# Kernel tuning notes

Hardware: AMD Instinct MI355X
Metric: run time of the kernel (lower is better)

Reference implementation:

```python
import jax, jax.numpy as jnp
import numpy as np

N_NODES = 50000


def gcn_conv(x, src, dst, deg_inv_sqrt, W, b, n_nodes):
    # GCNConv: h = x @ W; msg = norm * h[src]; out = scatter_add(msg, dst) + b
    h = x @ W  # [N, out]
    norm = deg_inv_sqrt[src] * deg_inv_sqrt[dst]  # symmetric normalization
    msg = h[src] * norm[:, None]  # [E+N, out]
    out = jax.ops.segment_sum(msg, dst, num_segments=n_nodes)
    return out + b


def setup_inputs() -> dict:
    key = jax.random.key(0)
    k_x, k_e, k_w1, k_w2 = jax.random.split(key, 4)
    in_c, hid, out_c = 256, 64, 64
    x = jax.random.normal(k_x, (N_NODES, 256), dtype=jnp.float32)
    edge_index = jax.random.randint(k_e, (2, 1600000), 0, N_NODES, dtype=jnp.int64)
    # Glorot-ish weights, zero bias as in GCNConv defaults
    W1 = jax.random.normal(k_w1, (in_c, hid), dtype=jnp.float32) / np.sqrt(in_c)
    b1 = jnp.zeros((hid,), dtype=jnp.float32)
    W2 = jax.random.normal(k_w2, (hid, out_c), dtype=jnp.float32) / np.sqrt(hid)
    b2 = jnp.zeros((out_c,), dtype=jnp.float32)
    return {"x": x, "edge_index": edge_index, "W1": W1, "b1": b1, "W2": W2, "b2": b2}


def reference(x, edge_index, W1, b1, W2, b2):
    n = x.shape[0]
    loops = jnp.arange(n, dtype=edge_index.dtype)
    src = jnp.concatenate([edge_index[0], loops])  # add self-loops
    dst = jnp.concatenate([edge_index[1], loops])
    deg = jax.ops.segment_sum(jnp.ones_like(dst, dtype=x.dtype), dst, num_segments=n)
    deg_inv_sqrt = jnp.where(deg > 0, jax.lax.rsqrt(deg), 0.0)
    h = gcn_conv(x, src, dst, deg_inv_sqrt, W1, b1, n)
    h = jax.nn.relu(h)
    out = gcn_conv(h, src, dst, deg_inv_sqrt, W2, b2, n)
    return out
```

## Files before the change

kernel.cpp:

```cpp
#include <hip/hip_runtime.h>
#include <hip/hip_bf16.h>


#define NB_MAX 1024

__device__ inline unsigned short f2bf(float f) {
    unsigned u = __builtin_bit_cast(unsigned, f);
    return (unsigned short)((u + 0x7FFFu + ((u >> 16) & 1u)) >> 16);
}
__device__ inline float bf2f(unsigned short b) {
    return __builtin_bit_cast(float, (unsigned)b << 16);
}


__global__ __launch_bounds__(256) void k_hist(const int* __restrict__ ei, int E,
                                              int nb, int chunk,
                                              int* __restrict__ histT) {
    __shared__ int h[NB_MAX];
    for (int i = threadIdx.x; i < nb; i += 256) h[i] = 0;
    __syncthreads();
    int e0 = blockIdx.x * chunk, e1 = min(E, e0 + chunk);
    for (int e = e0 + threadIdx.x; e < e1; e += 256)
        atomicAdd(&h[ei[E + e] >> 6], 1);
    __syncthreads();
    for (int b = threadIdx.x; b < nb; b += 256)
        histT[b * 256 + blockIdx.x] = h[b];
}


__global__ __launch_bounds__(256) void k_scan_cols(int* __restrict__ histT,
                                                   int* __restrict__ total) {
    __shared__ int sm[256];
    int b = blockIdx.x, t = threadIdx.x;
    int v = histT[b * 256 + t];
    sm[t] = v;
    __syncthreads();
    for (int off = 1; off < 256; off <<= 1) {
        int u = (t >= off) ? sm[t - off] : 0;
        __syncthreads();
        sm[t] += u;
        __syncthreads();
    }
    histT[b * 256 + t] = sm[t] - v;
    if (t == 255) total[b] = sm[255];
}


__global__ __launch_bounds__(1024) void k_scan_totals(const int* __restrict__ total,
                                                      int* __restrict__ base, int nb) {
    __shared__ int sm[1024];
    int t = threadIdx.x;
    int v = (t < nb) ? total[t] : 0;
    sm[t] = v;
    __syncthreads();
    for (int off = 1; off < 1024; off <<= 1) {
        int u = (t >= off) ? sm[t - off] : 0;
        __syncthreads();
        sm[t] += u;
        __syncthreads();
    }
    if (t < nb) base[t] = sm[t] - v;
    if (t == nb - 1) base[nb] = sm[t];
}


__global__ __launch_bounds__(256) void k_scatter(const int* __restrict__ ei, int E,
                                                 int nb, int chunk,
                                                 const int* __restrict__ histT,
                                                 const int* __restrict__ base,
                                                 unsigned* __restrict__ packed) {
    __shared__ int cur[NB_MAX];
    for (int b = threadIdx.x; b < nb; b += 256)
        cur[b] = base[b] + histT[b * 256 + blockIdx.x];
    __syncthreads();
    int e0 = blockIdx.x * chunk, e1 = min(E, e0 + chunk);
    for (int e = e0 + threadIdx.x; e < e1; e += 256) {
        int s = ei[e], d = ei[E + e];
        int pos = atomicAdd(&cur[d >> 6], 1);
        packed[pos] = (unsigned)s | ((unsigned)(d & 63) << 16);
    }
}


__global__ __launch_bounds__(256) void k_csr(const unsigned* __restrict__ packed,
                                             const int* __restrict__ base,
                                             int n,
                                             int* __restrict__ qbeg,
                                             int* __restrict__ qcnt,
                                             float* __restrict__ dinv,
                                             unsigned short* __restrict__ ssrcp,
                                             unsigned short* __restrict__ hs1,
                                             unsigned short* __restrict__ hs2) {
    __shared__ int cnt[64];
    __shared__ int cur[64];
    const int b = blockIdx.x, t = threadIdx.x;
    const int p0 = base[b], p1 = base[b + 1];
    if (t < 64) cnt[t] = 0;
    __syncthreads();
    for (int p = p0 + t; p < p1; p += 256)
        atomicAdd(&cnt[(packed[p] >> 16) & 63], 1);
    __syncthreads();
    if (t < 64) {
        int deg = cnt[t];
        int pdeg = (deg + 1) & ~1;
        int sum = pdeg;
#pragma unroll
        for (int d = 1; d < 64; d <<= 1) {
            int u = __shfl_up(sum, d, 64);
            if (t >= d) sum += u;
        }
        int excl = sum - pdeg;
        int pb = (2 + p0 + 128 * b + 1) & ~1;
        int start = pb + excl;
        int node = (b << 6) + t;
        if (node < n) {
            qbeg[node] = start >> 1;
            qcnt[node] = pdeg >> 1;
            dinv[node] = 1.0f / sqrtf((float)(deg + 1));
        }
        cur[t] = start;
    }
    __syncthreads();
    for (int p = p0 + t; p < p1; p += 256) {
        unsigned k = packed[p];
        int pos = atomicAdd(&cur[(k >> 16) & 63], 1);
        ssrcp[pos] = (unsigned short)(k & 0xFFFFu);
    }
    __syncthreads();
    if (t < 64 && (cnt[t] & 1))
        ssrcp[cur[t]] = (unsigned short)n;
    if (b == 0) {
        if (t < 64) {
            hs1[(size_t)n * 64 + t] = 0;
            hs2[(size_t)n * 64 + t] = 0;
        }
        if (t == 0) {
            ssrcp[0] = (unsigned short)n;
            ssrcp[1] = (unsigned short)n;
        }
    }
}


#define FMA4(A, s, wv)                                                         \
    (A).x += (s) * (wv).x; (A).y += (s) * (wv).y;                              \
    (A).z += (s) * (wv).z; (A).w += (s) * (wv).w;

template <int K>
__global__ __launch_bounds__(256) void k_gemm(const float* __restrict__ X,
                                              const float* __restrict__ W,
                                              const float* __restrict__ dinv,
                                              unsigned short* __restrict__ HS,
                                              int n) {
    __shared__ float xl[64][36];
    __shared__ float wl[32][64];

    const int t = threadIdx.x;
    const int tc = t & 15;
    const int tr = t >> 4;
    const int row0 = blockIdx.x * 64;

    float4 acc[4];
    acc[0] = acc[1] = acc[2] = acc[3] = make_float4(0.f, 0.f, 0.f, 0.f);

    for (int k0 = 0; k0 < K; k0 += 32) {
#pragma unroll
        for (int i = 0; i < 2; ++i) {
            int idx = i * 256 + t;
            int r = idx >> 3, f4 = idx & 7;
            int gr = row0 + r;
            float4 v = make_float4(0.f, 0.f, 0.f, 0.f);
            if (gr < n) v = *(const float4*)(X + (size_t)gr * K + k0 + f4 * 4);
            *(float4*)&xl[r][f4 * 4] = v;
        }
#pragma unroll
        for (int i = 0; i < 2; ++i) {
            int idx = i * 256 + t;
            int kr = idx >> 4, f4 = idx & 15;
            *(float4*)&wl[kr][f4 * 4] =
                *(const float4*)(W + (size_t)(k0 + kr) * 64 + f4 * 4);
        }
        __syncthreads();

#pragma unroll
        for (int kk = 0; kk < 32; kk += 4) {
            float4 xv0 = *(float4*)&xl[tr * 4 + 0][kk];
            float4 xv1 = *(float4*)&xl[tr * 4 + 1][kk];
            float4 xv2 = *(float4*)&xl[tr * 4 + 2][kk];
            float4 xv3 = *(float4*)&xl[tr * 4 + 3][kk];
            float4 wv0 = *(float4*)&wl[kk + 0][tc * 4];
            float4 wv1 = *(float4*)&wl[kk + 1][tc * 4];
            float4 wv2 = *(float4*)&wl[kk + 2][tc * 4];
            float4 wv3 = *(float4*)&wl[kk + 3][tc * 4];

            FMA4(acc[0], xv0.x, wv0); FMA4(acc[0], xv0.y, wv1);
            FMA4(acc[0], xv0.z, wv2); FMA4(acc[0], xv0.w, wv3);
            FMA4(acc[1], xv1.x, wv0); FMA4(acc[1], xv1.y, wv1);
            FMA4(acc[1], xv1.z, wv2); FMA4(acc[1], xv1.w, wv3);
            FMA4(acc[2], xv2.x, wv0); FMA4(acc[2], xv2.y, wv1);
            FMA4(acc[2], xv2.z, wv2); FMA4(acc[2], xv2.w, wv3);
            FMA4(acc[3], xv3.x, wv0); FMA4(acc[3], xv3.y, wv1);
            FMA4(acc[3], xv3.z, wv2); FMA4(acc[3], xv3.w, wv3);
        }
        __syncthreads();
    }

#pragma unroll
    for (int ri = 0; ri < 4; ++ri) {
        int gr = row0 + tr * 4 + ri;
        if (gr < n) {
            float dv = dinv[gr];
            float4 o = acc[ri];
            ushort4 pk;
            pk.x = f2bf(o.x * dv); pk.y = f2bf(o.y * dv);
            pk.z = f2bf(o.z * dv); pk.w = f2bf(o.w * dv);
            *(ushort4*)(HS + (size_t)gr * 64 + tc * 4) = pk;
        }
    }
}


template <bool RELU>
__global__ void k_agg(const unsigned short* __restrict__ hs,
                      const int* __restrict__ qbeg,
                      const int* __restrict__ qcnt,
                      const unsigned short* __restrict__ ssrcp,
                      const float* __restrict__ dinv,
                      const float* __restrict__ bias,
                      float* __restrict__ out, int n) {
    int node = blockIdx.x * 4 + (threadIdx.x >> 6);
    if (node >= n) return;
    node = __builtin_amdgcn_readfirstlane(node);
    const int lane = threadIdx.x & 63;
    const int half = lane >> 5;
    const int cp   = lane & 31;

    const unsigned* hsu = (const unsigned*)hs;
    const unsigned* ssu = (const unsigned*)ssrcp;

    const int q0 = qbeg[node];
    const int m  = qcnt[node];

    const unsigned sv = hsu[node * 32 + cp];
    const float dv = dinv[node];
    const float2 bv = *(const float2*)(bias + 2 * cp);

    float ax = 0.f, ay = 0.f;
    int qb = 0;
    for (; qb + 16 <= m; qb += 16) {
        unsigned ss[16];
#pragma unroll
        for (int j = 0; j < 16; ++j) ss[j] = ssu[q0 + qb + j];
        unsigned v[16];
#pragma unroll
        for (int j = 0; j < 16; ++j) {
            int s = half ? (int)(ss[j] >> 16) : (int)(ss[j] & 0xFFFFu);
            v[j] = hsu[s * 32 + cp];
        }
#pragma unroll
        for (int j = 0; j < 16; ++j) {
            ax += __builtin_bit_cast(float, v[j] << 16);
            ay += __builtin_bit_cast(float, v[j] & 0xFFFF0000u);
        }
    }
    const int rem = m - qb;
    if (rem) {
        unsigned ss[16];
#pragma unroll
        for (int j = 0; j < 16; ++j) {
            int q = (j < rem) ? (q0 + qb + j) : 0;
            ss[j] = ssu[q];
        }
        unsigned v[16];
#pragma unroll
        for (int j = 0; j < 16; ++j) {
            int s = half ? (int)(ss[j] >> 16) : (int)(ss[j] & 0xFFFFu);
            v[j] = hsu[s * 32 + cp];
        }
#pragma unroll
        for (int j = 0; j < 16; ++j) {
            ax += __builtin_bit_cast(float, v[j] << 16);
            ay += __builtin_bit_cast(float, v[j] & 0xFFFF0000u);
        }
    }

    ax += __shfl_xor(ax, 32, 64);
    ay += __shfl_xor(ay, 32, 64);

    float rx = dv * (ax + __builtin_bit_cast(float, sv << 16)) + bv.x;
    float ry = dv * (ay + __builtin_bit_cast(float, sv & 0xFFFF0000u)) + bv.y;
    if (RELU) { rx = fmaxf(rx, 0.f); ry = fmaxf(ry, 0.f); }
    if (half == 0)
        *(float2*)(out + (size_t)node * 64 + 2 * cp) = make_float2(rx, ry);
}


extern "C" void kernel_launch(void* const* d_in, const int* in_sizes, int n_in,
                              void* d_out, int out_size, void* d_ws, size_t ws_size,
                              hipStream_t stream) {
    const float* x  = (const float*)d_in[0];
    const int*   ei = (const int*)d_in[1];
    const float* W1 = (const float*)d_in[2];
    const float* b1 = (const float*)d_in[3];
    const float* W2 = (const float*)d_in[4];
    const float* b2 = (const float*)d_in[5];

    const int n = in_sizes[0] / 256;
    const int E = in_sizes[1] / 2;
    const int nb = (n + 63) >> 6;
    const int chunk = (E + 255) / 256;

    char* ws = (char*)d_ws;
    auto carve = [&](size_t bytes) {
        void* p = (void*)ws;
        ws += (bytes + 255) & ~(size_t)255;
        return p;
    };
    int*            histT  = (int*)carve((size_t)nb * 256 * 4);
    int*            total  = (int*)carve((size_t)nb * 4);
    int*            base   = (int*)carve((size_t)(nb + 1) * 4);
    unsigned*       packed = (unsigned*)carve((size_t)E * 4);
    unsigned short* ssrcp  = (unsigned short*)carve(((size_t)E + 128 * nb + 256) * 2);
    int*            qbeg   = (int*)carve((size_t)n * 4);
    int*            qcnt   = (int*)carve((size_t)n * 4);
    float*          dinv   = (float*)carve((size_t)n * 4);
    unsigned short* hs1    = (unsigned short*)carve((size_t)(n + 1) * 64 * 2);
    float*          hB     = (float*)carve((size_t)n * 64 * 4);
    unsigned short* hs2    = (unsigned short*)carve((size_t)(n + 1) * 64 * 2);

    k_hist<<<256, 256, 0, stream>>>(ei, E, nb, chunk, histT);
    k_scan_cols<<<nb, 256, 0, stream>>>(histT, total);
    k_scan_totals<<<1, 1024, 0, stream>>>(total, base, nb);
    k_scatter<<<256, 256, 0, stream>>>(ei, E, nb, chunk, histT, base, packed);
    k_csr<<<nb, 256, 0, stream>>>(packed, base, n, qbeg, qcnt, dinv, ssrcp,
                                  hs1, hs2);

    const int nbG = (n + 63) / 64;

    k_gemm<256><<<nbG, 256, 0, stream>>>(x, W1, dinv, hs1, n);
    k_agg<true><<<(n + 3) / 4, 256, 0, stream>>>(hs1, qbeg, qcnt, ssrcp, dinv,
                                                 b1, hB, n);

    k_gemm<64><<<nbG, 256, 0, stream>>>(hB, W2, dinv, hs2, n);
    k_agg<false><<<(n + 3) / 4, 256, 0, stream>>>(hs2, qbeg, qcnt, ssrcp, dinv,
                                                  b2, (float*)d_out, n);
}
```

Measured before the change: 227.4 us.

## Widen aggregation gathers to 16-byte rows, enlarge preprocessing blocks to 1024

The aggregation kernel now gathers a full 128-byte bf16 row with 8 lanes per edge, each lane loading 16 bytes. This handles 8 edges per wavefront iteration instead of 2 edges with 4-byte loads, and finishes with a three-step cross-lane reduction. The change is meant to cut the number of memory instructions and raise bytes per gather. The histogram, scatter and CSR kernels also move from 256 to 1024 threads per block, so each block has more parallelism. In exchange there are more registers per lane, extra shuffle reductions, and fewer active lanes on the final store.

```diff
diff --git a/kernel.cpp b/kernel.cpp
--- a/kernel.cpp
+++ b/kernel.cpp
@@ -8,22 +8,25 @@
     unsigned u = __builtin_bit_cast(unsigned, f);
     return (unsigned short)((u + 0x7FFFu + ((u >> 16) & 1u)) >> 16);
 }
-__device__ inline float bf2f(unsigned short b) {
-    return __builtin_bit_cast(float, (unsigned)b << 16);
-}
-
-
-__global__ __launch_bounds__(256) void k_hist(const int* __restrict__ ei, int E,
-                                              int nb, int chunk,
-                                              int* __restrict__ histT) {
+__device__ inline float blo(unsigned u) {
+    return __builtin_bit_cast(float, u << 16);
+}
+__device__ inline float bhi(unsigned u) {
+    return __builtin_bit_cast(float, u & 0xFFFF0000u);
+}
+
+
+__global__ __launch_bounds__(1024) void k_hist(const int* __restrict__ ei, int E,
+                                               int nb, int chunk,
+                                               int* __restrict__ histT) {
     __shared__ int h[NB_MAX];
-    for (int i = threadIdx.x; i < nb; i += 256) h[i] = 0;
+    for (int i = threadIdx.x; i < nb; i += 1024) h[i] = 0;
     __syncthreads();
     int e0 = blockIdx.x * chunk, e1 = min(E, e0 + chunk);
-    for (int e = e0 + threadIdx.x; e < e1; e += 256)
+    for (int e = e0 + threadIdx.x; e < e1; e += 1024)
         atomicAdd(&h[ei[E + e] >> 6], 1);
     __syncthreads();
-    for (int b = threadIdx.x; b < nb; b += 256)
+    for (int b = threadIdx.x; b < nb; b += 1024)
         histT[b * 256 + blockIdx.x] = h[b];
 }
 
@@ -64,17 +67,17 @@
 }
 
 
-__global__ __launch_bounds__(256) void k_scatter(const int* __restrict__ ei, int E,
-                                                 int nb, int chunk,
-                                                 const int* __restrict__ histT,
-                                                 const int* __restrict__ base,
-                                                 unsigned* __restrict__ packed) {
+__global__ __launch_bounds__(1024) void k_scatter(const int* __restrict__ ei, int E,
+                                                  int nb, int chunk,
+                                                  const int* __restrict__ histT,
+                                                  const int* __restrict__ base,
+                                                  unsigned* __restrict__ packed) {
     __shared__ int cur[NB_MAX];
-    for (int b = threadIdx.x; b < nb; b += 256)
+    for (int b = threadIdx.x; b < nb; b += 1024)
         cur[b] = base[b] + histT[b * 256 + blockIdx.x];
     __syncthreads();
     int e0 = blockIdx.x * chunk, e1 = min(E, e0 + chunk);
-    for (int e = e0 + threadIdx.x; e < e1; e += 256) {
+    for (int e = e0 + threadIdx.x; e < e1; e += 1024) {
         int s = ei[e], d = ei[E + e];
         int pos = atomicAdd(&cur[d >> 6], 1);
         packed[pos] = (unsigned)s | ((unsigned)(d & 63) << 16);
@@ -82,22 +85,22 @@
 }
 
 
-__global__ __launch_bounds__(256) void k_csr(const unsigned* __restrict__ packed,
-                                             const int* __restrict__ base,
-                                             int n,
-                                             int* __restrict__ qbeg,
-                                             int* __restrict__ qcnt,
-                                             float* __restrict__ dinv,
-                                             unsigned short* __restrict__ ssrcp,
-                                             unsigned short* __restrict__ hs1,
-                                             unsigned short* __restrict__ hs2) {
+__global__ __launch_bounds__(1024) void k_csr(const unsigned* __restrict__ packed,
+                                              const int* __restrict__ base,
+                                              int n,
+                                              int* __restrict__ qbeg,
+                                              int* __restrict__ qcnt,
+                                              float* __restrict__ dinv,
+                                              unsigned short* __restrict__ ssrcp,
+                                              unsigned short* __restrict__ hs1,
+                                              unsigned short* __restrict__ hs2) {
     __shared__ int cnt[64];
     __shared__ int cur[64];
     const int b = blockIdx.x, t = threadIdx.x;
     const int p0 = base[b], p1 = base[b + 1];
     if (t < 64) cnt[t] = 0;
     __syncthreads();
-    for (int p = p0 + t; p < p1; p += 256)
+    for (int p = p0 + t; p < p1; p += 1024)
         atomicAdd(&cnt[(packed[p] >> 16) & 63], 1);
     __syncthreads();
     if (t < 64) {
@@ -121,7 +124,7 @@
         cur[t] = start;
     }
     __syncthreads();
-    for (int p = p0 + t; p < p1; p += 256) {
+    for (int p = p0 + t; p < p1; p += 1024) {
         unsigned k = packed[p];
         int pos = atomicAdd(&cur[(k >> 16) & 63], 1);
         ssrcp[pos] = (unsigned short)(k & 0xFFFFu);
@@ -221,7 +224,7 @@
 
 
 template <bool RELU>
-__global__ void k_agg(const unsigned short* __restrict__ hs,
+__global__ __launch_bounds__(256) void k_agg(const unsigned short* __restrict__ hs,
                       const int* __restrict__ qbeg,
                       const int* __restrict__ qcnt,
                       const unsigned short* __restrict__ ssrcp,
@@ -232,66 +235,95 @@
     if (node >= n) return;
     node = __builtin_amdgcn_readfirstlane(node);
     const int lane = threadIdx.x & 63;
-    const int half = lane >> 5;
-    const int cp   = lane & 31;
-
-    const unsigned* hsu = (const unsigned*)hs;
+    const int c = lane & 7;
+    const int shH = (lane & 8) ? 16 : 0;
+
+    const uint4* hs4 = (const uint4*)hs;
     const unsigned* ssu = (const unsigned*)ssrcp;
 
     const int q0 = qbeg[node];
     const int m  = qcnt[node];
 
-    const unsigned sv = hsu[node * 32 + cp];
+    const uint4 sv = hs4[node * 8 + c];
     const float dv = dinv[node];
-    const float2 bv = *(const float2*)(bias + 2 * cp);
-
-    float ax = 0.f, ay = 0.f;
+    const float4 bv0 = *(const float4*)(bias + 8 * c);
+    const float4 bv1 = *(const float4*)(bias + 8 * c + 4);
+
+    float ax[8];
+#pragma unroll
+    for (int k = 0; k < 8; ++k) ax[k] = 0.f;
+
     int qb = 0;
-    for (; qb + 16 <= m; qb += 16) {
-        unsigned ss[16];
-#pragma unroll
-        for (int j = 0; j < 16; ++j) ss[j] = ssu[q0 + qb + j];
-        unsigned v[16];
-#pragma unroll
-        for (int j = 0; j < 16; ++j) {
-            int s = half ? (int)(ss[j] >> 16) : (int)(ss[j] & 0xFFFFu);
-            v[j] = hsu[s * 32 + cp];
-        }
-#pragma unroll
-        for (int j = 0; j < 16; ++j) {
-            ax += __builtin_bit_cast(float, v[j] << 16);
-            ay += __builtin_bit_cast(float, v[j] & 0xFFFF0000u);
+    for (; qb + 8 <= m; qb += 8) {
+        unsigned ssl[8];
+#pragma unroll
+        for (int j = 0; j < 8; ++j) ssl[j] = ssu[q0 + qb + j];
+        uint4 v[2];
+#pragma unroll
+        for (int i = 0; i < 2; ++i) {
+            unsigned w = (lane & 32) ? ((lane & 16) ? ssl[4 * i + 3] : ssl[4 * i + 2])
+                                     : ((lane & 16) ? ssl[4 * i + 1] : ssl[4 * i + 0]);
+            int s = (int)((w >> shH) & 0xFFFFu);
+            v[i] = hs4[s * 8 + c];
+        }
+#pragma unroll
+        for (int i = 0; i < 2; ++i) {
+            ax[0] += blo(v[i].x); ax[1] += bhi(v[i].x);
+            ax[2] += blo(v[i].y); ax[3] += bhi(v[i].y);
+            ax[4] += blo(v[i].z); ax[5] += bhi(v[i].z);
+            ax[6] += blo(v[i].w); ax[7] += bhi(v[i].w);
         }
     }
     const int rem = m - qb;
     if (rem) {
-        unsigned ss[16];
-#pragma unroll
-        for (int j = 0; j < 16; ++j) {
+        unsigned ssl[8];
+#pragma unroll
+        for (int j = 0; j < 8; ++j) {
             int q = (j < rem) ? (q0 + qb + j) : 0;
-            ss[j] = ssu[q];
-        }
-        unsigned v[16];
-#pragma unroll
-        for (int j = 0; j < 16; ++j) {
-            int s = half ? (int)(ss[j] >> 16) : (int)(ss[j] & 0xFFFFu);
-            v[j] = hsu[s * 32 + cp];
-        }
-#pragma unroll
-        for (int j = 0; j < 16; ++j) {
-            ax += __builtin_bit_cast(float, v[j] << 16);
-            ay += __builtin_bit_cast(float, v[j] & 0xFFFF0000u);
-        }
-    }
-
-    ax += __shfl_xor(ax, 32, 64);
-    ay += __shfl_xor(ay, 32, 64);
-
-    float rx = dv * (ax + __builtin_bit_cast(float, sv << 16)) + bv.x;
-    float ry = dv * (ay + __builtin_bit_cast(float, sv & 0xFFFF0000u)) + bv.y;
-    if (RELU) { rx = fmaxf(rx, 0.f); ry = fmaxf(ry, 0.f); }
-    if (half == 0)
-        *(float2*)(out + (size_t)node * 64 + 2 * cp) = make_float2(rx, ry);
+            ssl[j] = ssu[q];
+        }
+        uint4 v[2];
+#pragma unroll
+        for (int i = 0; i < 2; ++i) {
+            unsigned w = (lane & 32) ? ((lane & 16) ? ssl[4 * i + 3] : ssl[4 * i + 2])
+                                     : ((lane & 16) ? ssl[4 * i + 1] : ssl[4 * i + 0]);
+            int s = (int)((w >> shH) & 0xFFFFu);
+            v[i] = hs4[s * 8 + c];
+        }
+#pragma unroll
+        for (int i = 0; i < 2; ++i) {
+            ax[0] += blo(v[i].x); ax[1] += bhi(v[i].x);
+            ax[2] += blo(v[i].y); ax[3] += bhi(v[i].y);
+            ax[4] += blo(v[i].z); ax[5] += bhi(v[i].z);
+            ax[6] += blo(v[i].w); ax[7] += bhi(v[i].w);
+        }
+    }
+
+#pragma unroll
+    for (int k = 0; k < 8; ++k) {
+        ax[k] += __shfl_xor(ax[k], 8, 64);
+        ax[k] += __shfl_xor(ax[k], 16, 64);
+        ax[k] += __shfl_xor(ax[k], 32, 64);
+    }
+
+    float r[8];
+    r[0] = dv * (ax[0] + blo(sv.x)) + bv0.x;
+    r[1] = dv * (ax[1] + bhi(sv.x)) + bv0.y;
+    r[2] = dv * (ax[2] + blo(sv.y)) + bv0.z;
+    r[3] = dv * (ax[3] + bhi(sv.y)) + bv0.w;
+    r[4] = dv * (ax[4] + blo(sv.z)) + bv1.x;
+    r[5] = dv * (ax[5] + bhi(sv.z)) + bv1.y;
+    r[6] = dv * (ax[6] + blo(sv.w)) + bv1.z;
+    r[7] = dv * (ax[7] + bhi(sv.w)) + bv1.w;
+    if (RELU) {
+#pragma unroll
+        for (int k = 0; k < 8; ++k) r[k] = fmaxf(r[k], 0.f);
+    }
+    if (lane < 16) {
+        float4 o = (lane & 8) ? make_float4(r[4], r[5], r[6], r[7])
+                              : make_float4(r[0], r[1], r[2], r[3]);
+        *(float4*)(out + (size_t)node * 64 + 8 * c + 4 * ((lane >> 3) & 1)) = o;
+    }
 }
 
 
@@ -328,12 +360,12 @@
     float*          hB     = (float*)carve((size_t)n * 64 * 4);
     unsigned short* hs2    = (unsigned short*)carve((size_t)(n + 1) * 64 * 2);
 
-    k_hist<<<256, 256, 0, stream>>>(ei, E, nb, chunk, histT);
+    k_hist<<<256, 1024, 0, stream>>>(ei, E, nb, chunk, histT);
     k_scan_cols<<<nb, 256, 0, stream>>>(histT, total);
     k_scan_totals<<<1, 1024, 0, stream>>>(total, base, nb);
-    k_scatter<<<256, 256, 0, stream>>>(ei, E, nb, chunk, histT, base, packed);
-    k_csr<<<nb, 256, 0, stream>>>(packed, base, n, qbeg, qcnt, dinv, ssrcp,
-                                  hs1, hs2);
+    k_scatter<<<256, 1024, 0, stream>>>(ei, E, nb, chunk, histT, base, packed);
+    k_csr<<<nb, 1024, 0, stream>>>(packed, base, n, qbeg, qcnt, dinv, ssrcp,
+                                   hs1, hs2);
 
     const int nbG = (n + 63) / 64;
 
```

After: 215.6 us. 5.2% less time.
